# Kernel optimization log

Hardware: AMD Instinct MI355X
Metric: run time of the kernel (lower is better)

## Reference

```python
import jax, jax.numpy as jnp
import numpy as np

SIZES = [64, 64, 64, 64]
N_SAMPLES = 8192


def radialkernel(u, v):
    # exp(u.v^T - |u|^2/2 - |v|^2/2), shape [rows(u), rows(v)]
    uu = jnp.sum(u * u, axis=1, keepdims=True)
    vv = jnp.sum(v * v, axis=1, keepdims=True)
    return jnp.exp(u @ v.T - uu / 2 - vv.T / 2)


def setup_inputs() -> dict:
    key = jax.random.key(0)
    k0, k1, k2, k3 = jax.random.split(key, 4)
    d_in = 256
    total = sum(SIZES)            # 256
    rest = sum(SIZES[1:])         # 192
    data = jax.random.normal(k0, (N_SAMPLES, d_in), jnp.float32)
    inputs = jax.random.normal(k1, (2048, d_in), jnp.float32)
    # Linear(d_in, total): weight [total, d_in], bias [total]
    W = jax.random.normal(k2, (total, d_in), jnp.float32) / np.sqrt(d_in)
    b = jnp.zeros((total,), jnp.float32)
    # xavier_uniform for c_ss [N, rest]
    limit = np.sqrt(6.0 / (N_SAMPLES + rest)).astype(np.float32)
    c_ss = jax.random.uniform(k3, (N_SAMPLES, rest), jnp.float32, -limit, limit)
    return {"data": data, "inputs": inputs, "W": W, "b": b, "c_ss": c_ss}


def reference(data, inputs, W, b, c_ss):
    n = N_SAMPLES
    x = jnp.concatenate([data, inputs], axis=0) @ W.T + b  # [N+B, total]
    reg = jnp.sum(W * W) + jnp.sum(b * b)
    xss = list(jnp.split(x, np.cumsum(SIZES[:-1]), axis=1))
    css = jnp.split(c_ss, np.cumsum(SIZES[1:-1]), axis=1)
    ker = jnp.zeros((x.shape[0], n), x.dtype)
    for i, cs in enumerate(css):  # len(sizes)-1 iterations (small, fixed)
        xs = xss[i]
        ker = ker + radialkernel(xs, xs[:n])  # [N+B, N]
        val = ker @ cs                        # [N+B, sizes[i+1]]
        xss[i + 1] = xss[i + 1] + val
        reg = reg + jnp.sum(cs * val[:n])
    return xss[-1][n:], reg
```

## Files before the change

kernel.cpp:

```cpp
#include <hip/hip_runtime.h>
#include <hip/hip_bf16.h>

typedef unsigned short u16;
typedef unsigned int   u32;
typedef __attribute__((ext_vector_type(8)))  short bf16x8;
typedef __attribute__((ext_vector_type(16))) float f32x16;

#define N_S   8192
#define M_TOT 10240
#define SEGS  8
#define SEG   1024
#define QT    320

__device__ __forceinline__ u16 f2bf(float f) {
  u32 x = __float_as_uint(f);
  u32 r = x + 0x7FFFu + ((x >> 16) & 1u);
  return (u16)(r >> 16);
}
__device__ __forceinline__ float bf2f(u16 h) {
  return __uint_as_float(((u32)h) << 16);
}

__global__ __launch_bounds__(256) void gemm_x(const float* __restrict__ data,
                                              const float* __restrict__ inp,
                                              const float* __restrict__ W,
                                              const float* __restrict__ bias,
                                              float* __restrict__ x)
{
  __shared__ __align__(16) u16 At[64 * 256];
  __shared__ __align__(16) u16 Wt[64 * 256];
  const int t  = threadIdx.x;
  const int rb = blockIdx.x * 64, cb = blockIdx.y * 64;

#pragma unroll
  for (int it = 0; it < 8; ++it) {
    int c = it * 256 + t;
    int row = c >> 5, c8 = c & 31;
    int grow = rb + row;
    const float* src = (grow < N_S) ? data + (size_t)grow * 256 + c8 * 8
                                    : inp + (size_t)(grow - N_S) * 256 + c8 * 8;
    float4 v0 = *(const float4*)src;
    float4 v1 = *(const float4*)(src + 4);
    u16 h[8] = {f2bf(v0.x), f2bf(v0.y), f2bf(v0.z), f2bf(v0.w),
                f2bf(v1.x), f2bf(v1.y), f2bf(v1.z), f2bf(v1.w)};
    *(int4*)((char*)At + row * 512 + ((c8 * 16) ^ ((row & 7) << 4))) = *(int4*)h;

    const float* wsrc = W + (size_t)(cb + row) * 256 + c8 * 8;
    float4 w0 = *(const float4*)wsrc;
    float4 w1 = *(const float4*)(wsrc + 4);
    u16 g[8] = {f2bf(w0.x), f2bf(w0.y), f2bf(w0.z), f2bf(w0.w),
                f2bf(w1.x), f2bf(w1.y), f2bf(w1.z), f2bf(w1.w)};
    *(int4*)((char*)Wt + row * 512 + ((c8 * 16) ^ ((row & 7) << 4))) = *(int4*)g;
  }
  __syncthreads();

  const int w = t >> 6, lane = t & 63, l31 = lane & 31, hi = lane >> 5;
  const int wr = (w >> 1) * 32, wc = (w & 1) * 32;
  f32x16 acc;
#pragma unroll
  for (int r = 0; r < 16; ++r) acc[r] = 0.f;
  const char* Ab = (const char*)At + (size_t)(wr + l31) * 512;
  const char* Bb = (const char*)Wt + (size_t)(wc + l31) * 512;
  const int rx = (l31 & 7) << 4;
#pragma unroll
  for (int k0 = 0; k0 < 256; k0 += 16) {
    bf16x8 af = *(const bf16x8*)(Ab + ((k0 * 2 + hi * 16) ^ rx));
    bf16x8 bfv = *(const bf16x8*)(Bb + ((k0 * 2 + hi * 16) ^ rx));
    acc = __builtin_amdgcn_mfma_f32_32x32x16_bf16(af, bfv, acc, 0, 0, 0);
  }
  float bv = bias[cb + wc + l31];
#pragma unroll
  for (int r = 0; r < 16; ++r) {
    int qr = (r & 3) + 8 * (r >> 2) + 4 * hi;
    x[(size_t)(rb + wr + qr) * 256 + cb + wc + l31] = acc[r] + bv;
  }
}

__global__ __launch_bounds__(256) void prep_csT(const float* __restrict__ css,
                                                u16* __restrict__ csbT)
{
  __shared__ float tile[64][65];
  const int i  = blockIdx.y;
  const int r0 = blockIdx.x * 64;
  const int t  = threadIdx.x;
#pragma unroll
  for (int it = 0; it < 4; ++it) {
    int r  = (t >> 4) + it * 16;
    int c4 = (t & 15) * 4;
    float4 v = *(const float4*)(css + (size_t)(r0 + r) * 192 + i * 64 + c4);
    tile[r][c4] = v.x; tile[r][c4 + 1] = v.y; tile[r][c4 + 2] = v.z; tile[r][c4 + 3] = v.w;
  }
  __syncthreads();
  const int c = t >> 2, rq = (t & 3) * 16;
  u16 tmp[16];
#pragma unroll
  for (int e = 0; e < 16; ++e) tmp[e] = f2bf(tile[rq + e][c]);
  u16* dst = csbT + (size_t)i * (64 * (size_t)N_S) + (size_t)c * N_S + r0 + rq;
  *(int4*)dst       = *(int4*)tmp;
  *(int4*)(dst + 8) = *(int4*)(tmp + 8);
}

__global__ __launch_bounds__(256) void regw_ker(const float* __restrict__ W,
                                                const float* __restrict__ bias,
                                                float* __restrict__ regpart)
{
  __shared__ float red[256];
  const int t = threadIdx.x, b = blockIdx.x;
  float4 v = *(const float4*)(W + (size_t)b * 1024 + t * 4);
  float s = v.x * v.x + v.y * v.y + v.z * v.z + v.w * v.w;
  if (b == 0) { float bv = bias[t]; s += bv * bv; }
  red[t] = s; __syncthreads();
#pragma unroll
  for (int o = 128; o; o >>= 1) {
    if (t < o) red[t] += red[t + o];
    __syncthreads();
  }
  if (t == 0) regpart[b] = red[0];
}

__global__ __launch_bounds__(256) void prep_xb(const float* __restrict__ x, int j,
                                               u16* __restrict__ xbj, u32* __restrict__ hlj)
{
  const int w = threadIdx.x >> 6, lane = threadIdx.x & 63;
  const int row = blockIdx.x * 4 + w;
  float v = x[(size_t)row * 256 + (size_t)j * 64 + lane];
  u16 h = f2bf(v);
  float f = bf2f(h);
  xbj[(size_t)row * 64 + lane] = h;
  float s = f * f;
#pragma unroll
  for (int o = 32; o; o >>= 1) s += __shfl_xor(s, o);
  if (lane == 0) {
    float A  = 0.5f * s;
    u16  hq  = f2bf(A);
    u16  lq  = f2bf(A - bf2f(hq));
    hlj[row] = (u32)hq | ((u32)lq << 16);
  }
}

__global__ __launch_bounds__(64) void screen_ker(const u16* __restrict__ xbj,
                                                 const u32* __restrict__ hlj,
                                                 u32* __restrict__ maskj)
{
  const int lane = threadIdx.x & 63, l31 = lane & 31, hi = lane >> 5;
  const int qq  = blockIdx.x;
  const int seg = blockIdx.y;
  const int w   = blockIdx.z;

  bf16x8 qf[4][4];
  u32 hlq[4];
#pragma unroll
  for (int q = 0; q < 4; ++q) {
    const int qrow = (qq * 4 + q) * 32 + l31;
    const u16* qp = xbj + (size_t)qrow * 64 + hi * 8;
#pragma unroll
    for (int d = 0; d < 4; ++d) qf[q][d] = *(const bf16x8*)(qp + d * 16);
    hlq[q] = hlj[qrow];
  }

  f32x16 Z;
#pragma unroll
  for (int r = 0; r < 16; ++r) Z[r] = 0.f;

  u32 bits0 = 0, bits1 = 0, bits2 = 0, bits3 = 0;
  const int nt0 = seg * 32 + w * 8;
#pragma unroll
  for (int it = 0; it < 8; ++it) {
    const int nb = (nt0 + it) * 32;
    const u16* kp = xbj + (size_t)(nb + l31) * 64 + hi * 8;
    bf16x8 kf0 = *(const bf16x8*)(kp);
    bf16x8 kf1 = *(const bf16x8*)(kp + 16);
    bf16x8 kf2 = *(const bf16x8*)(kp + 32);
    bf16x8 kf3 = *(const bf16x8*)(kp + 48);
    u32 hlk = hlj[nb + l31];
    union { bf16x8 v; u32 d[4]; } ke;
    ke.d[0] = hi ? 0u : 0xBF80BF80u;
    ke.d[1] = hi ? 0u : (hlk ^ 0x80008000u);
    ke.d[2] = 0u; ke.d[3] = 0u;
#pragma unroll
    for (int q = 0; q < 4; ++q) {
      f32x16 S = __builtin_amdgcn_mfma_f32_32x32x16_bf16(qf[q][0], kf0, Z, 0, 0, 0);
      S = __builtin_amdgcn_mfma_f32_32x32x16_bf16(qf[q][1], kf1, S, 0, 0, 0);
      S = __builtin_amdgcn_mfma_f32_32x32x16_bf16(qf[q][2], kf2, S, 0, 0, 0);
      S = __builtin_amdgcn_mfma_f32_32x32x16_bf16(qf[q][3], kf3, S, 0, 0, 0);
      union { bf16x8 v; u32 d[4]; } qe;
      qe.d[0] = hi ? 0u : hlq[q];
      qe.d[1] = hi ? 0u : 0x3F803F80u;
      qe.d[2] = 0u; qe.d[3] = 0u;
      S = __builtin_amdgcn_mfma_f32_32x32x16_bf16(qe.v, ke.v, S, 0, 0, 0);
      float m0 = fmaxf(S[0], S[1]),  m1 = fmaxf(S[2], S[3]);
      float m2 = fmaxf(S[4], S[5]),  m3 = fmaxf(S[6], S[7]);
      float m4 = fmaxf(S[8], S[9]),  m5 = fmaxf(S[10], S[11]);
      float m6 = fmaxf(S[12], S[13]), m7 = fmaxf(S[14], S[15]);
      float mx = fmaxf(fmaxf(fmaxf(m0, m1), fmaxf(m2, m3)),
                       fmaxf(fmaxf(m4, m5), fmaxf(m6, m7)));
      u32 b = (__any(mx > -25.0f) ? 1u : 0u) << it;
      if (q == 0) bits0 |= b;
      else if (q == 1) bits1 |= b;
      else if (q == 2) bits2 |= b;
      else bits3 |= b;
    }
  }
  if (lane == 0) {
    unsigned char* mb = (unsigned char*)maskj;
    mb[((size_t)(qq * 4 + 0) * SEGS + seg) * 4 + w] = (unsigned char)bits0;
    mb[((size_t)(qq * 4 + 1) * SEGS + seg) * 4 + w] = (unsigned char)bits1;
    mb[((size_t)(qq * 4 + 2) * SEGS + seg) * 4 + w] = (unsigned char)bits2;
    mb[((size_t)(qq * 4 + 3) * SEGS + seg) * 4 + w] = (unsigned char)bits3;
  }
}

template<int NJ>
__global__ __launch_bounds__(256) void fused_ker(const u16* __restrict__ xb,
                                                 const u32* __restrict__ hl,
                                                 const u16* __restrict__ csbT,
                                                 float* __restrict__ val,
                                                 const u32* __restrict__ mask)
{
  __shared__ __align__(16) u16 Pt[4][32 * 32];

  const int t    = threadIdx.x;
  const int w    = t >> 6;
  const int lane = t & 63;
  const int l31  = lane & 31;
  const int hi   = lane >> 5;
  const int seg   = blockIdx.y;
  const int qtile = blockIdx.x * 4 + w;
  const int qrow  = qtile * 32 + l31;

  u32 m[NJ];
  u32 uni = 0;
#pragma unroll
  for (int j = 0; j < NJ; ++j) {
    m[j] = mask[((size_t)j * QT + qtile) * SEGS + seg];
    uni |= m[j];
  }
  if (!uni) return;

  float* vout = val + (size_t)seg * ((size_t)M_TOT * 64);

  bf16x8 qf[NJ][4];
  u32    hlq[NJ];
#pragma unroll
  for (int j = 0; j < NJ; ++j) {
    const u16* xbj = xb + (size_t)j * ((size_t)M_TOT * 64);
#pragma unroll
    for (int dk = 0; dk < 4; ++dk)
      qf[j][dk] = *(const bf16x8*)(xbj + (size_t)qrow * 64 + dk * 16 + hi * 8);
    hlq[j] = hl[j * M_TOT + qrow];
  }

  f32x16 acc0, acc1;
#pragma unroll
  for (int r = 0; r < 16; ++r) { acc0[r] = 0.f; acc1[r] = 0.f; }
  const int nb0 = seg * SEG;

  u32 rem = uni;
  while (rem) {
    const int nt = __ffs(rem) - 1;
    rem &= rem - 1;
    const int nb = nb0 + nt * 32;
    f32x16 P;
#pragma unroll
    for (int r = 0; r < 16; ++r) P[r] = 0.f;
#pragma unroll
    for (int j = 0; j < NJ; ++j) {
      if ((m[j] >> nt) & 1u) {
        const u16* xbj = xb + (size_t)j * ((size_t)M_TOT * 64);
        const u16* kp = xbj + (size_t)(nb + l31) * 64 + hi * 8;
        bf16x8 kf0 = *(const bf16x8*)(kp);
        bf16x8 kf1 = *(const bf16x8*)(kp + 16);
        bf16x8 kf2 = *(const bf16x8*)(kp + 32);
        bf16x8 kf3 = *(const bf16x8*)(kp + 48);
        u32 hlk = hl[j * M_TOT + nb + l31];
        f32x16 S;
#pragma unroll
        for (int r = 0; r < 16; ++r) S[r] = 0.f;
        S = __builtin_amdgcn_mfma_f32_32x32x16_bf16(qf[j][0], kf0, S, 0, 0, 0);
        S = __builtin_amdgcn_mfma_f32_32x32x16_bf16(qf[j][1], kf1, S, 0, 0, 0);
        S = __builtin_amdgcn_mfma_f32_32x32x16_bf16(qf[j][2], kf2, S, 0, 0, 0);
        S = __builtin_amdgcn_mfma_f32_32x32x16_bf16(qf[j][3], kf3, S, 0, 0, 0);
        union { bf16x8 v; u32 d[4]; } qe, ke;
        qe.d[0] = hi ? 0u : hlq[j];
        qe.d[1] = hi ? 0u : 0x3F803F80u;
        qe.d[2] = 0u; qe.d[3] = 0u;
        ke.d[0] = hi ? 0u : 0xBF80BF80u;
        ke.d[1] = hi ? 0u : (hlk ^ 0x80008000u);
        ke.d[2] = 0u; ke.d[3] = 0u;
        S = __builtin_amdgcn_mfma_f32_32x32x16_bf16(qe.v, ke.v, S, 0, 0, 0);
#pragma unroll
        for (int r = 0; r < 16; ++r) P[r] += __expf(S[r]);
      }
    }
    char* pw = (char*)&Pt[w][0];
#pragma unroll
    for (int r = 0; r < 16; ++r) {
      int qr = (r & 3) + 8 * (r >> 2) + 4 * hi;
      *(u16*)(pw + qr * 64 + ((l31 * 2) ^ ((qr & 3) << 4))) = f2bf(P[r]);
    }
    asm volatile("s_waitcnt lgkmcnt(0)" ::: "memory");
    bf16x8 pa0 = *(const bf16x8*)(pw + l31 * 64 + ((0  + hi * 16) ^ ((l31 & 3) << 4)));
    bf16x8 pa1 = *(const bf16x8*)(pw + l31 * 64 + ((32 + hi * 16) ^ ((l31 & 3) << 4)));
    asm volatile("s_waitcnt lgkmcnt(0)" ::: "memory");
    bf16x8 v00 = *(const bf16x8*)(csbT + (size_t)l31 * N_S + nb + hi * 8);
    bf16x8 v01 = *(const bf16x8*)(csbT + (size_t)l31 * N_S + nb + 16 + hi * 8);
    bf16x8 v10 = *(const bf16x8*)(csbT + (size_t)(32 + l31) * N_S + nb + hi * 8);
    bf16x8 v11 = *(const bf16x8*)(csbT + (size_t)(32 + l31) * N_S + nb + 16 + hi * 8);
    acc0 = __builtin_amdgcn_mfma_f32_32x32x16_bf16(pa0, v00, acc0, 0, 0, 0);
    acc0 = __builtin_amdgcn_mfma_f32_32x32x16_bf16(pa1, v01, acc0, 0, 0, 0);
    acc1 = __builtin_amdgcn_mfma_f32_32x32x16_bf16(pa0, v10, acc1, 0, 0, 0);
    acc1 = __builtin_amdgcn_mfma_f32_32x32x16_bf16(pa1, v11, acc1, 0, 0, 0);
  }

#pragma unroll
  for (int r = 0; r < 16; ++r) {
    int qr = (r & 3) + 8 * (r >> 2) + 4 * hi;
    size_t row = (size_t)(qtile * 32 + qr);
    vout[row * 64 + l31]      = acc0[r];
    vout[row * 64 + 32 + l31] = acc1[r];
  }
}

__global__ __launch_bounds__(256) void apply_ker(const float* __restrict__ val,
                                                 const float* __restrict__ css,
                                                 float* __restrict__ x, int i, int nj,
                                                 const u32* __restrict__ mask,
                                                 float* __restrict__ dotpart,
                                                 u16* __restrict__ xbn,
                                                 u32* __restrict__ hln)
{
  __shared__ float red[256];
  const int t = threadIdx.x;
  const int qtile = blockIdx.x;
  const int row = qtile * 32 + (t >> 3);
  const int coff = (t & 7) * 8;
  bool f[SEGS];
  bool anyf = false;
#pragma unroll
  for (int s = 0; s < SEGS; ++s) {
    u32 u = 0;
    for (int j = 0; j < nj; ++j) u |= mask[((size_t)j * QT + qtile) * SEGS + s];
    f[s] = (u != 0);
    anyf = anyf || f[s];
  }
  float v[8];
#pragma unroll
  for (int e = 0; e < 8; ++e) v[e] = 0.f;
  float dp = 0.f;
  float* xp = x + (size_t)row * 256 + (size_t)(i + 1) * 64 + coff;
  float4 xa = *(const float4*)xp;
  float4 xb4 = *(const float4*)(xp + 4);
  if (anyf) {
#pragma unroll
    for (int s = 0; s < SEGS; ++s) if (f[s]) {
      const float* vp = val + (size_t)s * ((size_t)M_TOT * 64) + (size_t)row * 64 + coff;
      float4 a = *(const float4*)vp;
      float4 b = *(const float4*)(vp + 4);
      v[0] += a.x; v[1] += a.y; v[2] += a.z; v[3] += a.w;
      v[4] += b.x; v[5] += b.y; v[6] += b.z; v[7] += b.w;
    }
    xa.x += v[0]; xa.y += v[1]; xa.z += v[2]; xa.w += v[3];
    xb4.x += v[4]; xb4.y += v[5]; xb4.z += v[6]; xb4.w += v[7];
    *(float4*)xp = xa;
    *(float4*)(xp + 4) = xb4;
    if (row < N_S) {
      const float* cp = css + (size_t)row * 192 + (size_t)i * 64 + coff;
      float4 ca = *(const float4*)cp;
      float4 cb = *(const float4*)(cp + 4);
      dp = ca.x * v[0] + ca.y * v[1] + ca.z * v[2] + ca.w * v[3]
         + cb.x * v[4] + cb.y * v[5] + cb.z * v[6] + cb.w * v[7];
    }
  }
  if (xbn) {
    float xv[8] = {xa.x, xa.y, xa.z, xa.w, xb4.x, xb4.y, xb4.z, xb4.w};
    u16 h[8];
    float s2 = 0.f;
#pragma unroll
    for (int e = 0; e < 8; ++e) {
      h[e] = f2bf(xv[e]);
      float fb = bf2f(h[e]);
      s2 += fb * fb;
    }
    *(int4*)(xbn + (size_t)row * 64 + coff) = *(int4*)h;
    s2 += __shfl_xor(s2, 1);
    s2 += __shfl_xor(s2, 2);
    s2 += __shfl_xor(s2, 4);
    if ((t & 7) == 0) {
      float A = 0.5f * s2;
      u16 hq = f2bf(A);
      u16 lq = f2bf(A - bf2f(hq));
      hln[row] = (u32)hq | ((u32)lq << 16);
    }
  }
  red[t] = dp; __syncthreads();
#pragma unroll
  for (int o = 128; o; o >>= 1) {
    if (t < o) red[t] += red[t + o];
    __syncthreads();
  }
  if (t == 0) dotpart[i * QT + qtile] = red[0];
}

__global__ __launch_bounds__(256) void final_ker(const float* __restrict__ x,
                                                 const float* __restrict__ regpart,
                                                 const float* __restrict__ dotpart,
                                                 float* __restrict__ out)
{
  if (blockIdx.x < 512) {
    int idx = blockIdx.x * 256 + threadIdx.x;
    int r = idx >> 6, c = idx & 63;
    out[idx] = x[(size_t)(N_S + r) * 256 + 192 + c];
    return;
  }
  __shared__ float red[256];
  float s = 0.f;
  for (int idx = threadIdx.x; idx < 3 * QT; idx += 256) s += dotpart[idx];
  if (threadIdx.x < 64) s += regpart[threadIdx.x];
  red[threadIdx.x] = s; __syncthreads();
#pragma unroll
  for (int o = 128; o; o >>= 1) {
    if (threadIdx.x < o) red[threadIdx.x] += red[threadIdx.x + o];
    __syncthreads();
  }
  if (threadIdx.x == 0) out[131072] = red[0];
}

extern "C" void kernel_launch(void* const* d_in, const int* in_sizes, int n_in,
                              void* d_out, int out_size, void* d_ws, size_t ws_size,
                              hipStream_t stream)
{
  const float* data = (const float*)d_in[0];
  const float* inp  = (const float*)d_in[1];
  const float* W    = (const float*)d_in[2];
  const float* bias = (const float*)d_in[3];
  const float* css  = (const float*)d_in[4];
  float* out = (float*)d_out;

  char* ws = (char*)d_ws;
  const size_t OFF_X    = 0;
  const size_t OFF_XB   = 10485760;
  const size_t OFF_HL   = OFF_XB + 3932160;
  const size_t OFF_CSBT = OFF_HL + 122880;
  const size_t OFF_VAL  = OFF_CSBT + 3145728;
  const size_t OFF_MASK = OFF_VAL + 20971520;
  const size_t OFF_REGW = OFF_MASK + 30720;
  const size_t OFF_DOT  = OFF_REGW + 256;

  float* x      = (float*)(ws + OFF_X);
  u16*   xb     = (u16*)  (ws + OFF_XB);
  u32*   hl     = (u32*)  (ws + OFF_HL);
  u16*   csbT   = (u16*)  (ws + OFF_CSBT);
  float* val    = (float*)(ws + OFF_VAL);
  u32*   mask   = (u32*)  (ws + OFF_MASK);
  float* regpart= (float*)(ws + OFF_REGW);
  float* dotpart= (float*)(ws + OFF_DOT);

  const size_t XB_STRIDE = (size_t)M_TOT * 64;
  const size_t CS_STRIDE = (size_t)64 * N_S;
  const size_t MK_STRIDE = (size_t)QT * SEGS;

  gemm_x   <<<dim3(160, 4), 256, 0, stream>>>(data, inp, W, bias, x);
  prep_csT <<<dim3(128, 3), 256, 0, stream>>>(css, csbT);
  regw_ker <<<64, 256, 0, stream>>>(W, bias, regpart);
  prep_xb  <<<2560, 256, 0, stream>>>(x, 0, xb, hl);
  screen_ker<<<dim3(80, SEGS, 4), 64, 0, stream>>>(xb, hl, mask);

  fused_ker<1><<<dim3(80, SEGS), 256, 0, stream>>>(xb, hl, csbT, val, mask);
  apply_ker<<<QT, 256, 0, stream>>>(val, css, x, 0, 1, mask, dotpart,
                                    xb + XB_STRIDE, hl + M_TOT);
  screen_ker<<<dim3(80, SEGS, 4), 64, 0, stream>>>(xb + XB_STRIDE, hl + M_TOT, mask + MK_STRIDE);

  fused_ker<2><<<dim3(80, SEGS), 256, 0, stream>>>(xb, hl, csbT + CS_STRIDE, val, mask);
  apply_ker<<<QT, 256, 0, stream>>>(val, css, x, 1, 2, mask, dotpart,
                                    xb + 2 * XB_STRIDE, hl + 2 * M_TOT);
  screen_ker<<<dim3(80, SEGS, 4), 64, 0, stream>>>(xb + 2 * XB_STRIDE, hl + 2 * M_TOT, mask + 2 * MK_STRIDE);

  fused_ker<3><<<dim3(80, SEGS), 256, 0, stream>>>(xb, hl, csbT + 2 * CS_STRIDE, val, mask);
  apply_ker<<<QT, 256, 0, stream>>>(val, css, x, 2, 3, mask, dotpart,
                                    (u16*)nullptr, (u32*)nullptr);

  final_ker<<<513, 256, 0, stream>>>(x, regpart, dotpart, out);
}
```

Baseline: 148.2 us.

## Fuse kernel-value, apply and bf16 prep into one per-tile mega kernel

```diff
diff --git a/kernel.cpp b/kernel.cpp
--- a/kernel.cpp
+++ b/kernel.cpp
@@ -25,10 +25,13 @@
                                               const float* __restrict__ inp,
                                               const float* __restrict__ W,
                                               const float* __restrict__ bias,
-                                              float* __restrict__ x)
+                                              float* __restrict__ x,
+                                              u16* __restrict__ xb0,
+                                              u32* __restrict__ hl0)
 {
   __shared__ __align__(16) u16 At[64 * 256];
   __shared__ __align__(16) u16 Wt[64 * 256];
+  __shared__ float part[64][2];
   const int t  = threadIdx.x;
   const int rb = blockIdx.x * 64, cb = blockIdx.y * 64;
 
@@ -74,6 +77,30 @@
     int qr = (r & 3) + 8 * (r >> 2) + 4 * hi;
     x[(size_t)(rb + wr + qr) * 256 + cb + wc + l31] = acc[r] + bv;
   }
+
+  if (cb == 0) {
+#pragma unroll
+    for (int r = 0; r < 16; ++r) {
+      int qr = (r & 3) + 8 * (r >> 2) + 4 * hi;
+      u16 h = f2bf(acc[r] + bv);
+      xb0[(size_t)(rb + wr + qr) * 64 + wc + l31] = h;
+      float fb = bf2f(h);
+      float s = fb * fb;
+      s += __shfl_xor(s, 1);
+      s += __shfl_xor(s, 2);
+      s += __shfl_xor(s, 4);
+      s += __shfl_xor(s, 8);
+      s += __shfl_xor(s, 16);
+      if (l31 == 0) part[wr + qr][w & 1] = s;
+    }
+    __syncthreads();
+    if (t < 64) {
+      float A = 0.5f * (part[t][0] + part[t][1]);
+      u16 hq = f2bf(A);
+      u16 lq = f2bf(A - bf2f(hq));
+      hl0[rb + t] = (u32)hq | ((u32)lq << 16);
+    }
+  }
 }
 
 __global__ __launch_bounds__(256) void prep_csT(const float* __restrict__ css,
@@ -116,26 +143,6 @@
     __syncthreads();
   }
   if (t == 0) regpart[b] = red[0];
-}
-
-__global__ __launch_bounds__(256) void prep_xb(const float* __restrict__ x, int j,
-                                               u16* __restrict__ xbj, u32* __restrict__ hlj)
-{
-  const int w = threadIdx.x >> 6, lane = threadIdx.x & 63;
-  const int row = blockIdx.x * 4 + w;
-  float v = x[(size_t)row * 256 + (size_t)j * 64 + lane];
-  u16 h = f2bf(v);
-  float f = bf2f(h);
-  xbj[(size_t)row * 64 + lane] = h;
-  float s = f * f;
-#pragma unroll
-  for (int o = 32; o; o >>= 1) s += __shfl_xor(s, o);
-  if (lane == 0) {
-    float A  = 0.5f * s;
-    u16  hq  = f2bf(A);
-    u16  lq  = f2bf(A - bf2f(hq));
-    hlj[row] = (u32)hq | ((u32)lq << 16);
-  }
 }
 
 __global__ __launch_bounds__(64) void screen_ker(const u16* __restrict__ xbj,
@@ -211,207 +218,175 @@
 }
 
 template<int NJ>
-__global__ __launch_bounds__(256) void fused_ker(const u16* __restrict__ xb,
-                                                 const u32* __restrict__ hl,
-                                                 const u16* __restrict__ csbT,
-                                                 float* __restrict__ val,
-                                                 const u32* __restrict__ mask)
-{
-  __shared__ __align__(16) u16 Pt[4][32 * 32];
-
-  const int t    = threadIdx.x;
-  const int w    = t >> 6;
-  const int lane = t & 63;
+__global__ __launch_bounds__(64) void mega_ker(const u16* __restrict__ xb,
+                                               const u32* __restrict__ hl,
+                                               const u16* __restrict__ csbT,
+                                               const u32* __restrict__ mask,
+                                               const float* __restrict__ css,
+                                               float* __restrict__ x,
+                                               float* __restrict__ dotpart,
+                                               u16* __restrict__ xbn,
+                                               u32* __restrict__ hln,
+                                               float* __restrict__ out)
+{
+  __shared__ __align__(16) u16 Pt[32 * 32];
+  const int lane = threadIdx.x & 63;
   const int l31  = lane & 31;
   const int hi   = lane >> 5;
-  const int seg   = blockIdx.y;
-  const int qtile = blockIdx.x * 4 + w;
+  const int qtile = blockIdx.x;
   const int qrow  = qtile * 32 + l31;
-
-  u32 m[NJ];
-  u32 uni = 0;
-#pragma unroll
-  for (int j = 0; j < NJ; ++j) {
-    m[j] = mask[((size_t)j * QT + qtile) * SEGS + seg];
-    uni |= m[j];
-  }
-  if (!uni) return;
-
-  float* vout = val + (size_t)seg * ((size_t)M_TOT * 64);
-
-  bf16x8 qf[NJ][4];
-  u32    hlq[NJ];
-#pragma unroll
-  for (int j = 0; j < NJ; ++j) {
-    const u16* xbj = xb + (size_t)j * ((size_t)M_TOT * 64);
-#pragma unroll
-    for (int dk = 0; dk < 4; ++dk)
-      qf[j][dk] = *(const bf16x8*)(xbj + (size_t)qrow * 64 + dk * 16 + hi * 8);
-    hlq[j] = hl[j * M_TOT + qrow];
+  constexpr int I = NJ - 1;
+
+  u32 m[NJ][SEGS];
+  u32 uni[SEGS];
+  u32 anyu = 0;
+#pragma unroll
+  for (int seg = 0; seg < SEGS; ++seg) {
+    u32 u = 0;
+#pragma unroll
+    for (int j = 0; j < NJ; ++j) {
+      m[j][seg] = mask[((size_t)j * QT + qtile) * SEGS + seg];
+      u |= m[j][seg];
+    }
+    uni[seg] = u;
+    anyu |= u;
   }
 
   f32x16 acc0, acc1;
 #pragma unroll
   for (int r = 0; r < 16; ++r) { acc0[r] = 0.f; acc1[r] = 0.f; }
-  const int nb0 = seg * SEG;
-
-  u32 rem = uni;
-  while (rem) {
-    const int nt = __ffs(rem) - 1;
-    rem &= rem - 1;
-    const int nb = nb0 + nt * 32;
-    f32x16 P;
-#pragma unroll
-    for (int r = 0; r < 16; ++r) P[r] = 0.f;
+
+  if (anyu) {
+    bf16x8 qf[NJ][4];
+    u32    hlq[NJ];
 #pragma unroll
     for (int j = 0; j < NJ; ++j) {
-      if ((m[j] >> nt) & 1u) {
-        const u16* xbj = xb + (size_t)j * ((size_t)M_TOT * 64);
-        const u16* kp = xbj + (size_t)(nb + l31) * 64 + hi * 8;
-        bf16x8 kf0 = *(const bf16x8*)(kp);
-        bf16x8 kf1 = *(const bf16x8*)(kp + 16);
-        bf16x8 kf2 = *(const bf16x8*)(kp + 32);
-        bf16x8 kf3 = *(const bf16x8*)(kp + 48);
-        u32 hlk = hl[j * M_TOT + nb + l31];
-        f32x16 S;
-#pragma unroll
-        for (int r = 0; r < 16; ++r) S[r] = 0.f;
-        S = __builtin_amdgcn_mfma_f32_32x32x16_bf16(qf[j][0], kf0, S, 0, 0, 0);
-        S = __builtin_amdgcn_mfma_f32_32x32x16_bf16(qf[j][1], kf1, S, 0, 0, 0);
-        S = __builtin_amdgcn_mfma_f32_32x32x16_bf16(qf[j][2], kf2, S, 0, 0, 0);
-        S = __builtin_amdgcn_mfma_f32_32x32x16_bf16(qf[j][3], kf3, S, 0, 0, 0);
-        union { bf16x8 v; u32 d[4]; } qe, ke;
-        qe.d[0] = hi ? 0u : hlq[j];
-        qe.d[1] = hi ? 0u : 0x3F803F80u;
-        qe.d[2] = 0u; qe.d[3] = 0u;
-        ke.d[0] = hi ? 0u : 0xBF80BF80u;
-        ke.d[1] = hi ? 0u : (hlk ^ 0x80008000u);
-        ke.d[2] = 0u; ke.d[3] = 0u;
-        S = __builtin_amdgcn_mfma_f32_32x32x16_bf16(qe.v, ke.v, S, 0, 0, 0);
-#pragma unroll
-        for (int r = 0; r < 16; ++r) P[r] += __expf(S[r]);
+      const u16* xbj = xb + (size_t)j * ((size_t)M_TOT * 64);
+#pragma unroll
+      for (int dk = 0; dk < 4; ++dk)
+        qf[j][dk] = *(const bf16x8*)(xbj + (size_t)qrow * 64 + dk * 16 + hi * 8);
+      hlq[j] = hl[j * M_TOT + qrow];
+    }
+
+#pragma unroll
+    for (int seg = 0; seg < SEGS; ++seg) {
+      u32 rem = uni[seg];
+      while (rem) {
+        const int nt = __ffs(rem) - 1;
+        rem &= rem - 1;
+        const int nb = seg * SEG + nt * 32;
+        f32x16 P;
+#pragma unroll
+        for (int r = 0; r < 16; ++r) P[r] = 0.f;
+#pragma unroll
+        for (int j = 0; j < NJ; ++j) {
+          if ((m[j][seg] >> nt) & 1u) {
+            const u16* xbj = xb + (size_t)j * ((size_t)M_TOT * 64);
+            const u16* kp = xbj + (size_t)(nb + l31) * 64 + hi * 8;
+            bf16x8 kf0 = *(const bf16x8*)(kp);
+            bf16x8 kf1 = *(const bf16x8*)(kp + 16);
+            bf16x8 kf2 = *(const bf16x8*)(kp + 32);
+            bf16x8 kf3 = *(const bf16x8*)(kp + 48);
+            u32 hlk = hl[j * M_TOT + nb + l31];
+            f32x16 S;
+#pragma unroll
+            for (int r = 0; r < 16; ++r) S[r] = 0.f;
+            S = __builtin_amdgcn_mfma_f32_32x32x16_bf16(qf[j][0], kf0, S, 0, 0, 0);
+            S = __builtin_amdgcn_mfma_f32_32x32x16_bf16(qf[j][1], kf1, S, 0, 0, 0);
+            S = __builtin_amdgcn_mfma_f32_32x32x16_bf16(qf[j][2], kf2, S, 0, 0, 0);
+            S = __builtin_amdgcn_mfma_f32_32x32x16_bf16(qf[j][3], kf3, S, 0, 0, 0);
+            union { bf16x8 v; u32 d[4]; } qe, ke;
+            qe.d[0] = hi ? 0u : hlq[j];
+            qe.d[1] = hi ? 0u : 0x3F803F80u;
+            qe.d[2] = 0u; qe.d[3] = 0u;
+            ke.d[0] = hi ? 0u : 0xBF80BF80u;
+            ke.d[1] = hi ? 0u : (hlk ^ 0x80008000u);
+            ke.d[2] = 0u; ke.d[3] = 0u;
+            S = __builtin_amdgcn_mfma_f32_32x32x16_bf16(qe.v, ke.v, S, 0, 0, 0);
+#pragma unroll
+            for (int r = 0; r < 16; ++r) P[r] += __expf(S[r]);
+          }
+        }
+        char* pw = (char*)Pt;
+#pragma unroll
+        for (int r = 0; r < 16; ++r) {
+          int qr = (r & 3) + 8 * (r >> 2) + 4 * hi;
+          *(u16*)(pw + qr * 64 + ((l31 * 2) ^ ((qr & 3) << 4))) = f2bf(P[r]);
+        }
+        asm volatile("s_waitcnt lgkmcnt(0)" ::: "memory");
+        bf16x8 pa0 = *(const bf16x8*)(pw + l31 * 64 + ((0  + hi * 16) ^ ((l31 & 3) << 4)));
+        bf16x8 pa1 = *(const bf16x8*)(pw + l31 * 64 + ((32 + hi * 16) ^ ((l31 & 3) << 4)));
+        asm volatile("s_waitcnt lgkmcnt(0)" ::: "memory");
+        bf16x8 v00 = *(const bf16x8*)(csbT + (size_t)l31 * N_S + nb + hi * 8);
+        bf16x8 v01 = *(const bf16x8*)(csbT + (size_t)l31 * N_S + nb + 16 + hi * 8);
+        bf16x8 v10 = *(const bf16x8*)(csbT + (size_t)(32 + l31) * N_S + nb + hi * 8);
+        bf16x8 v11 = *(const bf16x8*)(csbT + (size_t)(32 + l31) * N_S + nb + 16 + hi * 8);
+        acc0 = __builtin_amdgcn_mfma_f32_32x32x16_bf16(pa0, v00, acc0, 0, 0, 0);
+        acc0 = __builtin_amdgcn_mfma_f32_32x32x16_bf16(pa1, v01, acc0, 0, 0, 0);
+        acc1 = __builtin_amdgcn_mfma_f32_32x32x16_bf16(pa0, v10, acc1, 0, 0, 0);
+        acc1 = __builtin_amdgcn_mfma_f32_32x32x16_bf16(pa1, v11, acc1, 0, 0, 0);
       }
     }
-    char* pw = (char*)&Pt[w][0];
+  }
+
+  float dp = 0.f;
+  if (NJ < 3) {
 #pragma unroll
     for (int r = 0; r < 16; ++r) {
       int qr = (r & 3) + 8 * (r >> 2) + 4 * hi;
-      *(u16*)(pw + qr * 64 + ((l31 * 2) ^ ((qr & 3) << 4))) = f2bf(P[r]);
-    }
-    asm volatile("s_waitcnt lgkmcnt(0)" ::: "memory");
-    bf16x8 pa0 = *(const bf16x8*)(pw + l31 * 64 + ((0  + hi * 16) ^ ((l31 & 3) << 4)));
-    bf16x8 pa1 = *(const bf16x8*)(pw + l31 * 64 + ((32 + hi * 16) ^ ((l31 & 3) << 4)));
-    asm volatile("s_waitcnt lgkmcnt(0)" ::: "memory");
-    bf16x8 v00 = *(const bf16x8*)(csbT + (size_t)l31 * N_S + nb + hi * 8);
-    bf16x8 v01 = *(const bf16x8*)(csbT + (size_t)l31 * N_S + nb + 16 + hi * 8);
-    bf16x8 v10 = *(const bf16x8*)(csbT + (size_t)(32 + l31) * N_S + nb + hi * 8);
-    bf16x8 v11 = *(const bf16x8*)(csbT + (size_t)(32 + l31) * N_S + nb + 16 + hi * 8);
-    acc0 = __builtin_amdgcn_mfma_f32_32x32x16_bf16(pa0, v00, acc0, 0, 0, 0);
-    acc0 = __builtin_amdgcn_mfma_f32_32x32x16_bf16(pa1, v01, acc0, 0, 0, 0);
-    acc1 = __builtin_amdgcn_mfma_f32_32x32x16_bf16(pa0, v10, acc1, 0, 0, 0);
-    acc1 = __builtin_amdgcn_mfma_f32_32x32x16_bf16(pa1, v11, acc1, 0, 0, 0);
-  }
-
-#pragma unroll
-  for (int r = 0; r < 16; ++r) {
-    int qr = (r & 3) + 8 * (r >> 2) + 4 * hi;
-    size_t row = (size_t)(qtile * 32 + qr);
-    vout[row * 64 + l31]      = acc0[r];
-    vout[row * 64 + 32 + l31] = acc1[r];
-  }
-}
-
-__global__ __launch_bounds__(256) void apply_ker(const float* __restrict__ val,
-                                                 const float* __restrict__ css,
-                                                 float* __restrict__ x, int i, int nj,
-                                                 const u32* __restrict__ mask,
-                                                 float* __restrict__ dotpart,
-                                                 u16* __restrict__ xbn,
-                                                 u32* __restrict__ hln)
-{
-  __shared__ float red[256];
-  const int t = threadIdx.x;
-  const int qtile = blockIdx.x;
-  const int row = qtile * 32 + (t >> 3);
-  const int coff = (t & 7) * 8;
-  bool f[SEGS];
-  bool anyf = false;
-#pragma unroll
-  for (int s = 0; s < SEGS; ++s) {
-    u32 u = 0;
-    for (int j = 0; j < nj; ++j) u |= mask[((size_t)j * QT + qtile) * SEGS + s];
-    f[s] = (u != 0);
-    anyf = anyf || f[s];
-  }
-  float v[8];
-#pragma unroll
-  for (int e = 0; e < 8; ++e) v[e] = 0.f;
-  float dp = 0.f;
-  float* xp = x + (size_t)row * 256 + (size_t)(i + 1) * 64 + coff;
-  float4 xa = *(const float4*)xp;
-  float4 xb4 = *(const float4*)(xp + 4);
-  if (anyf) {
-#pragma unroll
-    for (int s = 0; s < SEGS; ++s) if (f[s]) {
-      const float* vp = val + (size_t)s * ((size_t)M_TOT * 64) + (size_t)row * 64 + coff;
-      float4 a = *(const float4*)vp;
-      float4 b = *(const float4*)(vp + 4);
-      v[0] += a.x; v[1] += a.y; v[2] += a.z; v[3] += a.w;
-      v[4] += b.x; v[5] += b.y; v[6] += b.z; v[7] += b.w;
-    }
-    xa.x += v[0]; xa.y += v[1]; xa.z += v[2]; xa.w += v[3];
-    xb4.x += v[4]; xb4.y += v[5]; xb4.z += v[6]; xb4.w += v[7];
-    *(float4*)xp = xa;
-    *(float4*)(xp + 4) = xb4;
-    if (row < N_S) {
-      const float* cp = css + (size_t)row * 192 + (size_t)i * 64 + coff;
-      float4 ca = *(const float4*)cp;
-      float4 cb = *(const float4*)(cp + 4);
-      dp = ca.x * v[0] + ca.y * v[1] + ca.z * v[2] + ca.w * v[3]
-         + cb.x * v[4] + cb.y * v[5] + cb.z * v[6] + cb.w * v[7];
-    }
-  }
-  if (xbn) {
-    float xv[8] = {xa.x, xa.y, xa.z, xa.w, xb4.x, xb4.y, xb4.z, xb4.w};
-    u16 h[8];
-    float s2 = 0.f;
-#pragma unroll
-    for (int e = 0; e < 8; ++e) {
-      h[e] = f2bf(xv[e]);
-      float fb = bf2f(h[e]);
-      s2 += fb * fb;
-    }
-    *(int4*)(xbn + (size_t)row * 64 + coff) = *(int4*)h;
-    s2 += __shfl_xor(s2, 1);
-    s2 += __shfl_xor(s2, 2);
-    s2 += __shfl_xor(s2, 4);
-    if ((t & 7) == 0) {
-      float A = 0.5f * s2;
-      u16 hq = f2bf(A);
-      u16 lq = f2bf(A - bf2f(hq));
-      hln[row] = (u32)hq | ((u32)lq << 16);
-    }
-  }
-  red[t] = dp; __syncthreads();
-#pragma unroll
-  for (int o = 128; o; o >>= 1) {
-    if (t < o) red[t] += red[t + o];
-    __syncthreads();
-  }
-  if (t == 0) dotpart[i * QT + qtile] = red[0];
-}
-
-__global__ __launch_bounds__(256) void final_ker(const float* __restrict__ x,
-                                                 const float* __restrict__ regpart,
+      int row = qtile * 32 + qr;
+      float* xp = x + (size_t)row * 256 + (size_t)(I + 1) * 64;
+      float n0 = xp[l31]      + acc0[r];
+      float n1 = xp[32 + l31] + acc1[r];
+      if (anyu) { xp[l31] = n0; xp[32 + l31] = n1; }
+      if (row < N_S) {
+        const float* cp = css + (size_t)row * 192 + (size_t)I * 64;
+        dp += cp[l31] * acc0[r] + cp[32 + l31] * acc1[r];
+      }
+      u16 h0 = f2bf(n0), h1 = f2bf(n1);
+      xbn[(size_t)row * 64 + l31]      = h0;
+      xbn[(size_t)row * 64 + 32 + l31] = h1;
+      float fb0 = bf2f(h0), fb1 = bf2f(h1);
+      float s = fb0 * fb0 + fb1 * fb1;
+      s += __shfl_xor(s, 1);
+      s += __shfl_xor(s, 2);
+      s += __shfl_xor(s, 4);
+      s += __shfl_xor(s, 8);
+      s += __shfl_xor(s, 16);
+      if (l31 == 0) {
+        float A = 0.5f * s;
+        u16 hq = f2bf(A);
+        u16 lq = f2bf(A - bf2f(hq));
+        hln[row] = (u32)hq | ((u32)lq << 16);
+      }
+    }
+  } else {
+#pragma unroll
+    for (int r = 0; r < 16; ++r) {
+      int qr = (r & 3) + 8 * (r >> 2) + 4 * hi;
+      int row = qtile * 32 + qr;
+      if (row < N_S) {
+        const float* cp = css + (size_t)row * 192 + (size_t)I * 64;
+        dp += cp[l31] * acc0[r] + cp[32 + l31] * acc1[r];
+      } else {
+        const float* xp = x + (size_t)row * 256 + 192;
+        float n0 = xp[l31]      + acc0[r];
+        float n1 = xp[32 + l31] + acc1[r];
+        float* op = out + (size_t)(row - N_S) * 64;
+        op[l31]      = n0;
+        op[32 + l31] = n1;
+      }
+    }
+  }
+#pragma unroll
+  for (int off = 32; off; off >>= 1) dp += __shfl_xor(dp, off);
+  if (lane == 0) dotpart[I * QT + qtile] = dp;
+}
+
+__global__ __launch_bounds__(256) void final_ker(const float* __restrict__ regpart,
                                                  const float* __restrict__ dotpart,
                                                  float* __restrict__ out)
 {
-  if (blockIdx.x < 512) {
-    int idx = blockIdx.x * 256 + threadIdx.x;
-    int r = idx >> 6, c = idx & 63;
-    out[idx] = x[(size_t)(N_S + r) * 256 + 192 + c];
-    return;
-  }
   __shared__ float red[256];
   float s = 0.f;
   for (int idx = threadIdx.x; idx < 3 * QT; idx += 256) s += dotpart[idx];
@@ -441,8 +416,7 @@
   const size_t OFF_XB   = 10485760;
   const size_t OFF_HL   = OFF_XB + 3932160;
   const size_t OFF_CSBT = OFF_HL + 122880;
-  const size_t OFF_VAL  = OFF_CSBT + 3145728;
-  const size_t OFF_MASK = OFF_VAL + 20971520;
+  const size_t OFF_MASK = OFF_CSBT + 3145728;
   const size_t OFF_REGW = OFF_MASK + 30720;
   const size_t OFF_DOT  = OFF_REGW + 256;
 
@@ -450,7 +424,6 @@
   u16*   xb     = (u16*)  (ws + OFF_XB);
   u32*   hl     = (u32*)  (ws + OFF_HL);
   u16*   csbT   = (u16*)  (ws + OFF_CSBT);
-  float* val    = (float*)(ws + OFF_VAL);
   u32*   mask   = (u32*)  (ws + OFF_MASK);
   float* regpart= (float*)(ws + OFF_REGW);
   float* dotpart= (float*)(ws + OFF_DOT);
@@ -459,25 +432,21 @@
   const size_t CS_STRIDE = (size_t)64 * N_S;
   const size_t MK_STRIDE = (size_t)QT * SEGS;
 
-  gemm_x   <<<dim3(160, 4), 256, 0, stream>>>(data, inp, W, bias, x);
+  gemm_x   <<<dim3(160, 4), 256, 0, stream>>>(data, inp, W, bias, x, xb, hl);
   prep_csT <<<dim3(128, 3), 256, 0, stream>>>(css, csbT);
   regw_ker <<<64, 256, 0, stream>>>(W, bias, regpart);
-  prep_xb  <<<2560, 256, 0, stream>>>(x, 0, xb, hl);
   screen_ker<<<dim3(80, SEGS, 4), 64, 0, stream>>>(xb, hl, mask);
 
-  fused_ker<1><<<dim3(80, SEGS), 256, 0, stream>>>(xb, hl, csbT, val, mask);
-  apply_ker<<<QT, 256, 0, stream>>>(val, css, x, 0, 1, mask, dotpart,
-                                    xb + XB_STRIDE, hl + M_TOT);
+  mega_ker<1><<<QT, 64, 0, stream>>>(xb, hl, csbT, mask, css, x, dotpart,
+                                     xb + XB_STRIDE, hl + M_TOT, (float*)nullptr);
   screen_ker<<<dim3(80, SEGS, 4), 64, 0, stream>>>(xb + XB_STRIDE, hl + M_TOT, mask + MK_STRIDE);
 
-  fused_ker<2><<<dim3(80, SEGS), 256, 0, stream>>>(xb, hl, csbT + CS_STRIDE, val, mask);
-  apply_ker<<<QT, 256, 0, stream>>>(val, css, x, 1, 2, mask, dotpart,
-                                    xb + 2 * XB_STRIDE, hl + 2 * M_TOT);
+  mega_ker<2><<<QT, 64, 0, stream>>>(xb, hl, csbT + CS_STRIDE, mask, css, x, dotpart,
+                                     xb + 2 * XB_STRIDE, hl + 2 * M_TOT, (float*)nullptr);
   screen_ker<<<dim3(80, SEGS, 4), 64, 0, stream>>>(xb + 2 * XB_STRIDE, hl + 2 * M_TOT, mask + 2 * MK_STRIDE);
 
-  fused_ker<3><<<dim3(80, SEGS), 256, 0, stream>>>(xb, hl, csbT + 2 * CS_STRIDE, val, mask);
-  apply_ker<<<QT, 256, 0, stream>>>(val, css, x, 2, 3, mask, dotpart,
-                                    (u16*)nullptr, (u32*)nullptr);
-
-  final_ker<<<513, 256, 0, stream>>>(x, regpart, dotpart, out);
-}
+  mega_ker<3><<<QT, 64, 0, stream>>>(xb, hl, csbT + 2 * CS_STRIDE, mask, css, x, dotpart,
+                                     (u16*)nullptr, (u32*)nullptr, out);
+
+  final_ker<<<1, 256, 0, stream>>>(regpart, dotpart, out);
+}
```

Result: slower. 226.3 us (+52.7%).

## Fuse prep_xb into gemm_x, widen screen grid, write output from apply

Applied to the files above, without the earlier changes.

```diff
diff --git a/kernel.cpp b/kernel.cpp
--- a/kernel.cpp
+++ b/kernel.cpp
@@ -25,10 +25,13 @@
                                               const float* __restrict__ inp,
                                               const float* __restrict__ W,
                                               const float* __restrict__ bias,
-                                              float* __restrict__ x)
+                                              float* __restrict__ x,
+                                              u16* __restrict__ xb0,
+                                              u32* __restrict__ hl0)
 {
   __shared__ __align__(16) u16 At[64 * 256];
   __shared__ __align__(16) u16 Wt[64 * 256];
+  __shared__ float part[64][2];
   const int t  = threadIdx.x;
   const int rb = blockIdx.x * 64, cb = blockIdx.y * 64;
 
@@ -74,6 +77,30 @@
     int qr = (r & 3) + 8 * (r >> 2) + 4 * hi;
     x[(size_t)(rb + wr + qr) * 256 + cb + wc + l31] = acc[r] + bv;
   }
+
+  if (cb == 0) {
+#pragma unroll
+    for (int r = 0; r < 16; ++r) {
+      int qr = (r & 3) + 8 * (r >> 2) + 4 * hi;
+      u16 h = f2bf(acc[r] + bv);
+      xb0[(size_t)(rb + wr + qr) * 64 + wc + l31] = h;
+      float fb = bf2f(h);
+      float s = fb * fb;
+      s += __shfl_xor(s, 1);
+      s += __shfl_xor(s, 2);
+      s += __shfl_xor(s, 4);
+      s += __shfl_xor(s, 8);
+      s += __shfl_xor(s, 16);
+      if (l31 == 0) part[wr + qr][w & 1] = s;
+    }
+    __syncthreads();
+    if (t < 64) {
+      float A = 0.5f * (part[t][0] + part[t][1]);
+      u16 hq = f2bf(A);
+      u16 lq = f2bf(A - bf2f(hq));
+      hl0[rb + t] = (u32)hq | ((u32)lq << 16);
+    }
+  }
 }
 
 __global__ __launch_bounds__(256) void prep_csT(const float* __restrict__ css,
@@ -118,26 +145,6 @@
   if (t == 0) regpart[b] = red[0];
 }
 
-__global__ __launch_bounds__(256) void prep_xb(const float* __restrict__ x, int j,
-                                               u16* __restrict__ xbj, u32* __restrict__ hlj)
-{
-  const int w = threadIdx.x >> 6, lane = threadIdx.x & 63;
-  const int row = blockIdx.x * 4 + w;
-  float v = x[(size_t)row * 256 + (size_t)j * 64 + lane];
-  u16 h = f2bf(v);
-  float f = bf2f(h);
-  xbj[(size_t)row * 64 + lane] = h;
-  float s = f * f;
-#pragma unroll
-  for (int o = 32; o; o >>= 1) s += __shfl_xor(s, o);
-  if (lane == 0) {
-    float A  = 0.5f * s;
-    u16  hq  = f2bf(A);
-    u16  lq  = f2bf(A - bf2f(hq));
-    hlj[row] = (u32)hq | ((u32)lq << 16);
-  }
-}
-
 __global__ __launch_bounds__(64) void screen_ker(const u16* __restrict__ xbj,
                                                  const u32* __restrict__ hlj,
                                                  u32* __restrict__ maskj)
@@ -162,10 +169,10 @@
 #pragma unroll
   for (int r = 0; r < 16; ++r) Z[r] = 0.f;
 
-  u32 bits0 = 0, bits1 = 0, bits2 = 0, bits3 = 0;
-  const int nt0 = seg * 32 + w * 8;
-#pragma unroll
-  for (int it = 0; it < 8; ++it) {
+  u32 bits[4] = {0u, 0u, 0u, 0u};
+  const int nt0 = seg * 32 + w * 4;
+#pragma unroll
+  for (int it = 0; it < 4; ++it) {
     const int nb = (nt0 + it) * 32;
     const u16* kp = xbj + (size_t)(nb + l31) * 64 + hi * 8;
     bf16x8 kf0 = *(const bf16x8*)(kp);
@@ -194,19 +201,13 @@
       float m6 = fmaxf(S[12], S[13]), m7 = fmaxf(S[14], S[15]);
       float mx = fmaxf(fmaxf(fmaxf(m0, m1), fmaxf(m2, m3)),
                        fmaxf(fmaxf(m4, m5), fmaxf(m6, m7)));
-      u32 b = (__any(mx > -25.0f) ? 1u : 0u) << it;
-      if (q == 0) bits0 |= b;
-      else if (q == 1) bits1 |= b;
-      else if (q == 2) bits2 |= b;
-      else bits3 |= b;
+      bits[q] |= (__any(mx > -25.0f) ? 1u : 0u) << it;
     }
   }
   if (lane == 0) {
-    unsigned char* mb = (unsigned char*)maskj;
-    mb[((size_t)(qq * 4 + 0) * SEGS + seg) * 4 + w] = (unsigned char)bits0;
-    mb[((size_t)(qq * 4 + 1) * SEGS + seg) * 4 + w] = (unsigned char)bits1;
-    mb[((size_t)(qq * 4 + 2) * SEGS + seg) * 4 + w] = (unsigned char)bits2;
-    mb[((size_t)(qq * 4 + 3) * SEGS + seg) * 4 + w] = (unsigned char)bits3;
+#pragma unroll
+    for (int q = 0; q < 4; ++q)
+      if (bits[q]) atomicOr(&maskj[(size_t)(qq * 4 + q) * SEGS + seg], bits[q] << (w * 4));
   }
 }
 
@@ -327,7 +328,8 @@
                                                  const u32* __restrict__ mask,
                                                  float* __restrict__ dotpart,
                                                  u16* __restrict__ xbn,
-                                                 u32* __restrict__ hln)
+                                                 u32* __restrict__ hln,
+                                                 float* __restrict__ out)
 {
   __shared__ float red[256];
   const int t = threadIdx.x;
@@ -359,10 +361,6 @@
       v[0] += a.x; v[1] += a.y; v[2] += a.z; v[3] += a.w;
       v[4] += b.x; v[5] += b.y; v[6] += b.z; v[7] += b.w;
     }
-    xa.x += v[0]; xa.y += v[1]; xa.z += v[2]; xa.w += v[3];
-    xb4.x += v[4]; xb4.y += v[5]; xb4.z += v[6]; xb4.w += v[7];
-    *(float4*)xp = xa;
-    *(float4*)(xp + 4) = xb4;
     if (row < N_S) {
       const float* cp = css + (size_t)row * 192 + (size_t)i * 64 + coff;
       float4 ca = *(const float4*)cp;
@@ -370,6 +368,18 @@
       dp = ca.x * v[0] + ca.y * v[1] + ca.z * v[2] + ca.w * v[3]
          + cb.x * v[4] + cb.y * v[5] + cb.z * v[6] + cb.w * v[7];
     }
+  }
+  xa.x += v[0]; xa.y += v[1]; xa.z += v[2]; xa.w += v[3];
+  xb4.x += v[4]; xb4.y += v[5]; xb4.z += v[6]; xb4.w += v[7];
+  if (i < 2) {
+    if (anyf) {
+      *(float4*)xp = xa;
+      *(float4*)(xp + 4) = xb4;
+    }
+  } else if (row >= N_S) {
+    float* op = out + (size_t)(row - N_S) * 64 + coff;
+    *(float4*)op = xa;
+    *(float4*)(op + 4) = xb4;
   }
   if (xbn) {
     float xv[8] = {xa.x, xa.y, xa.z, xa.w, xb4.x, xb4.y, xb4.z, xb4.w};
@@ -401,17 +411,10 @@
   if (t == 0) dotpart[i * QT + qtile] = red[0];
 }
 
-__global__ __launch_bounds__(256) void final_ker(const float* __restrict__ x,
-                                                 const float* __restrict__ regpart,
+__global__ __launch_bounds__(256) void final_ker(const float* __restrict__ regpart,
                                                  const float* __restrict__ dotpart,
                                                  float* __restrict__ out)
 {
-  if (blockIdx.x < 512) {
-    int idx = blockIdx.x * 256 + threadIdx.x;
-    int r = idx >> 6, c = idx & 63;
-    out[idx] = x[(size_t)(N_S + r) * 256 + 192 + c];
-    return;
-  }
   __shared__ float red[256];
   float s = 0.f;
   for (int idx = threadIdx.x; idx < 3 * QT; idx += 256) s += dotpart[idx];
@@ -459,25 +462,25 @@
   const size_t CS_STRIDE = (size_t)64 * N_S;
   const size_t MK_STRIDE = (size_t)QT * SEGS;
 
-  gemm_x   <<<dim3(160, 4), 256, 0, stream>>>(data, inp, W, bias, x);
+  hipMemsetAsync(mask, 0, 3 * MK_STRIDE * sizeof(u32), stream);
+  gemm_x   <<<dim3(160, 4), 256, 0, stream>>>(data, inp, W, bias, x, xb, hl);
   prep_csT <<<dim3(128, 3), 256, 0, stream>>>(css, csbT);
   regw_ker <<<64, 256, 0, stream>>>(W, bias, regpart);
-  prep_xb  <<<2560, 256, 0, stream>>>(x, 0, xb, hl);
-  screen_ker<<<dim3(80, SEGS, 4), 64, 0, stream>>>(xb, hl, mask);
+  screen_ker<<<dim3(80, SEGS, 8), 64, 0, stream>>>(xb, hl, mask);
 
   fused_ker<1><<<dim3(80, SEGS), 256, 0, stream>>>(xb, hl, csbT, val, mask);
   apply_ker<<<QT, 256, 0, stream>>>(val, css, x, 0, 1, mask, dotpart,
-                                    xb + XB_STRIDE, hl + M_TOT);
-  screen_ker<<<dim3(80, SEGS, 4), 64, 0, stream>>>(xb + XB_STRIDE, hl + M_TOT, mask + MK_STRIDE);
+                                    xb + XB_STRIDE, hl + M_TOT, (float*)nullptr);
+  screen_ker<<<dim3(80, SEGS, 8), 64, 0, stream>>>(xb + XB_STRIDE, hl + M_TOT, mask + MK_STRIDE);
 
   fused_ker<2><<<dim3(80, SEGS), 256, 0, stream>>>(xb, hl, csbT + CS_STRIDE, val, mask);
   apply_ker<<<QT, 256, 0, stream>>>(val, css, x, 1, 2, mask, dotpart,
-                                    xb + 2 * XB_STRIDE, hl + 2 * M_TOT);
-  screen_ker<<<dim3(80, SEGS, 4), 64, 0, stream>>>(xb + 2 * XB_STRIDE, hl + 2 * M_TOT, mask + 2 * MK_STRIDE);
+                                    xb + 2 * XB_STRIDE, hl + 2 * M_TOT, (float*)nullptr);
+  screen_ker<<<dim3(80, SEGS, 8), 64, 0, stream>>>(xb + 2 * XB_STRIDE, hl + 2 * M_TOT, mask + 2 * MK_STRIDE);
 
   fused_ker<3><<<dim3(80, SEGS), 256, 0, stream>>>(xb, hl, csbT + 2 * CS_STRIDE, val, mask);
   apply_ker<<<QT, 256, 0, stream>>>(val, css, x, 2, 3, mask, dotpart,
-                                    (u16*)nullptr, (u32*)nullptr);
-
-  final_ker<<<513, 256, 0, stream>>>(x, regpart, dotpart, out);
-}
+                                    (u16*)nullptr, (u32*)nullptr, out);
+
+  final_ker<<<1, 256, 0, stream>>>(regpart, dotpart, out);
+}
```

After: 157.7 us. +6.4%, slower.
